# Kernel tuning notes

Measured on AMD Instinct MI355X. Metric: run time of the kernel, lower is better.

## Reference

```python
import jax, jax.numpy as jnp
import numpy as np

N = 100000      # nodes
E = 640000      # directed edges (before self-loops)
F_IN = 128      # num_features
C1 = 64         # latent_size (conv1 out, heads=1)
C2 = 16         # num_classes (conv2 out, heads=1)
NEG_SLOPE = 0.2


def setup_inputs() -> dict:
    key = jax.random.key(0)
    ks = jax.random.split(key, 10)
    s = 0.1
    return {
        "x": jax.random.normal(ks[0], (N, F_IN), jnp.float32),
        "edge_index": jax.random.randint(ks[1], (2, E), 0, N, dtype=jnp.int32),
        "W1": jax.random.normal(ks[2], (F_IN, C1), jnp.float32) * s,
        "att_src1": jax.random.normal(ks[3], (C1,), jnp.float32) * s,
        "att_dst1": jax.random.normal(ks[4], (C1,), jnp.float32) * s,
        "b1": jax.random.normal(ks[5], (C1,), jnp.float32) * s,
        "W2": jax.random.normal(ks[6], (C1, C2), jnp.float32) * s,
        "att_src2": jax.random.normal(ks[7], (C2,), jnp.float32) * s,
        "att_dst2": jax.random.normal(ks[8], (C2,), jnp.float32) * s,
        "b2": jax.random.normal(ks[9], (C2,), jnp.float32) * s,
    }


def gat_layer(x, src, dst, W, a_src, a_dst, b, n_nodes):
    # x: [N, F] -> h: [N, C] (heads=1)
    h = x @ W
    # per-edge attention logits: alpha_j + alpha_i, then leaky_relu
    alpha = jax.nn.leaky_relu((h @ a_src)[src] + (h @ a_dst)[dst], NEG_SLOPE)
    # scatter-softmax over destination-node groups (numerically stable)
    amax = jax.ops.segment_max(alpha, dst, num_segments=n_nodes)
    e = jnp.exp(alpha - amax[dst])
    denom = jax.ops.segment_sum(e, dst, num_segments=n_nodes)
    w = e / (denom[dst] + 1e-16)
    # gather src features, weight, scatter-add to dst
    out = jax.ops.segment_sum(h[src] * w[:, None], dst, num_segments=n_nodes)
    return out + b


def kl_to_std_normal(out):
    # GIB reparameterize: mean = out[:, :ceil(C/2)], std = softplus(out[:, -ceil(C/2):])
    size = (out.shape[-1] + 1) // 2
    mean = out[:, :size]
    std = jax.nn.softplus(out[:, -size:]) + 1e-10
    kl = -jnp.log(std) + 0.5 * (std * std + mean * mean - 1.0)
    return kl.reshape(out.shape[0], -1, 1)  # [N, size, heads=1]


def reference(x, edge_index, W1, att_src1, att_dst1, b1, W2, att_src2, att_dst2, b2):
    n = x.shape[0]
    loop = jnp.arange(n, dtype=edge_index.dtype)  # PyG GATConv add_self_loops=True
    src = jnp.concatenate([edge_index[0], loop])
    dst = jnp.concatenate([edge_index[1], loop])

    out1 = gat_layer(x, src, dst, W1, att_src1, att_dst1, b1, n)
    ixz1 = kl_to_std_normal(out1)

    h = jax.nn.elu(out1)  # dropout is a no-op in eval mode
    out2 = gat_layer(h, src, dst, W2, att_src2, att_dst2, b2, n)
    ixz2 = kl_to_std_normal(out2)

    return (out2, ixz1, ixz2)
```

## Files before the change

kernel.cpp:

```cpp
#include <hip/hip_runtime.h>
#include <math.h>

#define NN 100000
#define NE 640000
#define FIN 128
#define C1 64
#define C2 16
#define NEG_SLOPE 0.2f
#define SLOTS 32
#define G1_BLOCKS ((NN + 127) / 128)
#define SORT_EPB 2048
#define SORT_NBLK ((NE + SORT_EPB - 1) / SORT_EPB)
#define NBUCK 512
#define NBUCK_USED ((NN + 255) / 256)

typedef unsigned int uint32;
typedef __attribute__((ext_vector_type(8))) short bf16x8;
typedef __attribute__((ext_vector_type(4))) float f32x4;

static __device__ __forceinline__ float lrelu(float x) { return x > 0.f ? x : NEG_SLOPE * x; }
static __device__ __forceinline__ float softplusn(float x) {
    return fmaxf(x, 0.f) + __logf(1.f + __expf(-fabsf(x)));
}
static __device__ __forceinline__ unsigned short f2bf(float f) {
    uint32 u = __float_as_uint(f);
    u += 0x7fffu + ((u >> 16) & 1u);
    return (unsigned short)(u >> 16);
}
static __device__ __forceinline__ float bf2f_lo(uint32 p) { return __uint_as_float(p << 16); }
static __device__ __forceinline__ float bf2f_hi(uint32 p) { return __uint_as_float(p & 0xffff0000u); }

#define G1T 2
__global__ __launch_bounds__(256, 3) void k_gemm1(
        const float* __restrict__ x, const float* __restrict__ W1,
        const float* __restrict__ attS, const float* __restrict__ attD,
        unsigned short* __restrict__ h1b, float* __restrict__ as1, float* __restrict__ ad1) {
    __shared__ uint32 ts[4][16][36];
    int lane = threadIdx.x & 63;
    int wv = threadIdx.x >> 6;
    int col = lane & 15;
    int g = lane >> 4;
    int wbase = (blockIdx.x * 4 + wv) * (G1T * 16);
    if (wbase >= NN) return;

    bf16x8 bfr[4][4];
#pragma unroll
    for (int t = 0; t < 4; t++)
#pragma unroll
        for (int j = 0; j < 4; j++) {
            int c = col + j * 16;
#pragma unroll
            for (int i = 0; i < 8; i++)
                bfr[t][j][i] = (short)f2bf(W1[(t * 32 + g * 8 + i) * C1 + c]);
        }
    float ats[4], atd[4];
#pragma unroll
    for (int j = 0; j < 4; j++) { ats[j] = attS[col + j * 16]; atd[j] = attD[col + j * 16]; }

    for (int tl = 0; tl < G1T; tl++) {
        int tbase = wbase + tl * 16;
        int arow = tbase + col; if (arow > NN - 1) arow = NN - 1;
        const float* xr = &x[(size_t)arow * FIN];
        float4 f0[4], f1[4];
#pragma unroll
        for (int t = 0; t < 4; t++) {
            f0[t] = *reinterpret_cast<const float4*>(&xr[t * 32 + g * 8]);
            f1[t] = *reinterpret_cast<const float4*>(&xr[t * 32 + g * 8 + 4]);
        }
        bf16x8 a[4];
#pragma unroll
        for (int t = 0; t < 4; t++) {
            a[t][0] = (short)f2bf(f0[t].x); a[t][1] = (short)f2bf(f0[t].y);
            a[t][2] = (short)f2bf(f0[t].z); a[t][3] = (short)f2bf(f0[t].w);
            a[t][4] = (short)f2bf(f1[t].x); a[t][5] = (short)f2bf(f1[t].y);
            a[t][6] = (short)f2bf(f1[t].z); a[t][7] = (short)f2bf(f1[t].w);
        }
        f32x4 acc[4];
#pragma unroll
        for (int j = 0; j < 4; j++) acc[j] = (f32x4){0.f, 0.f, 0.f, 0.f};
#pragma unroll
        for (int t = 0; t < 4; t++)
#pragma unroll
            for (int j = 0; j < 4; j++)
                acc[j] = __builtin_amdgcn_mfma_f32_16x16x32_bf16(a[t], bfr[t][j], acc[j], 0, 0, 0);

        float sA[4] = {0.f, 0.f, 0.f, 0.f}, sD[4] = {0.f, 0.f, 0.f, 0.f};
        unsigned short* tsw = (unsigned short*)&ts[wv][0][0];
#pragma unroll
        for (int reg = 0; reg < 4; reg++) {
            int trow = g * 4 + reg;
#pragma unroll
            for (int j = 0; j < 4; j++) {
                float v = acc[j][reg];
                tsw[trow * 72 + col + j * 16] = f2bf(v);
                sA[reg] = fmaf(v, ats[j], sA[reg]);
                sD[reg] = fmaf(v, atd[j], sD[reg]);
            }
        }
        __builtin_amdgcn_wave_barrier();
        {
            int rrow = lane >> 2, rq = lane & 3;
            uint4 w0 = *reinterpret_cast<const uint4*>(&ts[wv][rrow][rq * 8]);
            uint4 w1 = *reinterpret_cast<const uint4*>(&ts[wv][rrow][rq * 8 + 4]);
            int orow = tbase + rrow;
            if (orow < NN) {
                unsigned short* op = &h1b[(size_t)orow * C1 + rq * 16];
                *reinterpret_cast<uint4*>(op) = w0;
                *reinterpret_cast<uint4*>(op + 8) = w1;
            }
        }
        __builtin_amdgcn_wave_barrier();
#pragma unroll
        for (int off = 8; off; off >>= 1)
#pragma unroll
            for (int reg = 0; reg < 4; reg++) {
                sA[reg] += __shfl_xor(sA[reg], off);
                sD[reg] += __shfl_xor(sD[reg], off);
            }
        if (col == 0) {
#pragma unroll
            for (int reg = 0; reg < 4; reg++) {
                int row = tbase + g * 4 + reg;
                if (row < NN) { as1[row] = sA[reg]; ad1[row] = sD[reg]; }
            }
        }
    }
}

__global__ __launch_bounds__(256) void k_hist(const int* __restrict__ ei, int* __restrict__ blockHist) {
    __shared__ int lh[NBUCK];
    int t = threadIdx.x;
    for (int i = t; i < NBUCK; i += 256) lh[i] = 0;
    __syncthreads();
    int base = blockIdx.x * SORT_EPB;
#pragma unroll
    for (int k = 0; k < 8; k++) {
        int e = base + k * 256 + t;
        if (e < NE) atomicAdd(&lh[ei[NE + e] >> 8], 1);
    }
    __syncthreads();
    for (int i = t; i < NBUCK; i += 256) blockHist[i * SORT_NBLK + blockIdx.x] = lh[i];
}

__global__ __launch_bounds__(256) void k_scan(int* __restrict__ blockHist, int* __restrict__ bucketCnt) {
    __shared__ int s[SORT_NBLK];
    int b = blockIdx.x, t = threadIdx.x;
    for (int i = t; i < SORT_NBLK; i += 256) s[i] = blockHist[b * SORT_NBLK + i];
    __syncthreads();
    for (int d = 1; d < SORT_NBLK; d <<= 1) {
        int i0 = t, i1 = t + 256;
        int v0 = 0, v1 = 0;
        if (i0 >= d && i0 < SORT_NBLK) v0 = s[i0 - d];
        if (i1 >= d && i1 < SORT_NBLK) v1 = s[i1 - d];
        __syncthreads();
        if (i0 >= d && i0 < SORT_NBLK) s[i0] += v0;
        if (i1 >= d && i1 < SORT_NBLK) s[i1] += v1;
        __syncthreads();
    }
    for (int i = t; i < SORT_NBLK; i += 256)
        blockHist[b * SORT_NBLK + i] = (i == 0) ? 0 : s[i - 1];
    if (t == 0) bucketCnt[b] = s[SORT_NBLK - 1];
}

__global__ __launch_bounds__(256) void k_scat1(const int* __restrict__ ei,
        const int* __restrict__ blockHist, uint2* __restrict__ ebuf) {
    __shared__ int lh[NBUCK];
    int t = threadIdx.x;
    for (int i = t; i < NBUCK; i += 256) lh[i] = 0;
    __syncthreads();
    int base = blockIdx.x * SORT_EPB;
#pragma unroll
    for (int k = 0; k < 8; k++) {
        int e = base + k * 256 + t;
        if (e < NE) {
            int src = ei[e], dst = ei[NE + e];
            int bin = dst >> 8;
            int rank = atomicAdd(&lh[bin], 1);
            int pos = bin * SORT_EPB + blockHist[bin * SORT_NBLK + blockIdx.x] + rank;
            ebuf[pos] = make_uint2((uint32)src, (uint32)dst);
        }
    }
}

__global__ __launch_bounds__(256) void k_csr(const uint2* __restrict__ ebuf,
        const int* __restrict__ bucketCnt, int* __restrict__ cnt, int* __restrict__ csr32) {
    __shared__ int lcnt[256];
    __shared__ int lcsr[256 * SLOTS];
    int t = threadIdx.x, b = blockIdx.x;
    if (t < 256) lcnt[t] = 0;
    for (int i = t; i < 256 * SLOTS; i += 256) lcsr[i] = 0;
    __syncthreads();
    int n = bucketCnt[b];
    if (n > SORT_EPB) n = SORT_EPB;
    for (int i = t; i < n; i += 256) {
        uint2 e = ebuf[b * SORT_EPB + i];
        int ln = (int)(e.y & 255u);
        int pos = atomicAdd(&lcnt[ln], 1);
        if (pos < SLOTS) lcsr[ln * SLOTS + pos] = (int)e.x;
    }
    __syncthreads();
    int node0 = b * 256;
    for (int i = t; i < 256 * SLOTS; i += 256) {
        int node = node0 + (i >> 5);
        if (node < NN) csr32[(size_t)node0 * SLOTS + i] = lcsr[i];
    }
    if (node0 + t < NN) cnt[node0 + t] = lcnt[t];
}

__global__ __launch_bounds__(256, 4) void k_agg1(
        const int* __restrict__ cnt, const int* __restrict__ csr32,
        const float* __restrict__ as1, const float* __restrict__ ad1,
        const unsigned short* __restrict__ h1b, const float* __restrict__ b1,
        unsigned short* __restrict__ heb, float* __restrict__ ixz1) {
    int lane = threadIdx.x & 63;
    int wid = (blockIdx.x * blockDim.x + threadIdx.x) >> 6;
    int grp = lane >> 4, gl = lane & 15;
    int gbase = grp << 4;
    int node = wid * 4 + grp;
    if (node >= NN) return;
    int base = node * SLOTS;
    int dcnt = cnt[node];
    int s_l = csr32[base + gl];
    int4 S0 = *reinterpret_cast<const int4*>(&csr32[base]);
    int4 S1 = *reinterpret_cast<const int4*>(&csr32[base + 4]);
    int4 S2 = *reinterpret_cast<const int4*>(&csr32[base + 8]);
    int4 S3 = *reinterpret_cast<const int4*>(&csr32[base + 12]);
    float adn = ad1[node];
    float asn = as1[node];
    float asv = as1[s_l];
    float4 o;

    if (dcnt <= 16) {
        float al = (gl < dcnt) ? lrelu(asv + adn) : -1e30f;
        float wl = __expf(al);
        float den = wl;
#pragma unroll
        for (int off = 8; off; off >>= 1) den += __shfl_xor(den, off);
        float wself = __expf(lrelu(asn + adn));
        den += wself;
        float inv = __builtin_amdgcn_rcpf(den + 1e-16f);
        wl *= inv; wself *= inv;
        const unsigned short* hb = h1b + gl * 4;
        uint2 PS  = *reinterpret_cast<const uint2*>(&hb[(size_t)node * C1]);
        uint2 P0  = *reinterpret_cast<const uint2*>(&hb[(size_t)S0.x * C1]);
        uint2 P1  = *reinterpret_cast<const uint2*>(&hb[(size_t)S0.y * C1]);
        uint2 P2  = *reinterpret_cast<const uint2*>(&hb[(size_t)S0.z * C1]);
        uint2 P3  = *reinterpret_cast<const uint2*>(&hb[(size_t)S0.w * C1]);
        uint2 P4  = *reinterpret_cast<const uint2*>(&hb[(size_t)S1.x * C1]);
        uint2 P5  = *reinterpret_cast<const uint2*>(&hb[(size_t)S1.y * C1]);
        uint2 P6  = *reinterpret_cast<const uint2*>(&hb[(size_t)S1.z * C1]);
        uint2 P7  = *reinterpret_cast<const uint2*>(&hb[(size_t)S1.w * C1]);
        uint2 P8  = *reinterpret_cast<const uint2*>(&hb[(size_t)S2.x * C1]);
        uint2 P9  = *reinterpret_cast<const uint2*>(&hb[(size_t)S2.y * C1]);
        uint2 P10 = *reinterpret_cast<const uint2*>(&hb[(size_t)S2.z * C1]);
        uint2 P11 = *reinterpret_cast<const uint2*>(&hb[(size_t)S2.w * C1]);
        uint2 P12 = *reinterpret_cast<const uint2*>(&hb[(size_t)S3.x * C1]);
        uint2 P13 = *reinterpret_cast<const uint2*>(&hb[(size_t)S3.y * C1]);
        uint2 P14 = *reinterpret_cast<const uint2*>(&hb[(size_t)S3.z * C1]);
        uint2 P15 = *reinterpret_cast<const uint2*>(&hb[(size_t)S3.w * C1]);
        float4 acc;
        acc.x = wself * bf2f_lo(PS.x);
        acc.y = wself * bf2f_hi(PS.x);
        acc.z = wself * bf2f_lo(PS.y);
        acc.w = wself * bf2f_hi(PS.y);
#define ACC1(k, Pk) { float w = __shfl(wl, gbase | k); \
        acc.x = fmaf(w, bf2f_lo(Pk.x), acc.x); acc.y = fmaf(w, bf2f_hi(Pk.x), acc.y); \
        acc.z = fmaf(w, bf2f_lo(Pk.y), acc.z); acc.w = fmaf(w, bf2f_hi(Pk.y), acc.w); }
        ACC1(0, P0)  ACC1(1, P1)  ACC1(2, P2)  ACC1(3, P3)
        ACC1(4, P4)  ACC1(5, P5)  ACC1(6, P6)  ACC1(7, P7)
        ACC1(8, P8)  ACC1(9, P9)  ACC1(10, P10) ACC1(11, P11)
        ACC1(12, P12) ACC1(13, P13) ACC1(14, P14) ACC1(15, P15)
#undef ACC1
        o = acc;
    } else {
        int dcl = dcnt < SLOTS ? dcnt : SLOTS;
        float aself = lrelu(asn + adn);
        float m = aself;
        for (int e = gl; e < dcl; e += 16) m = fmaxf(m, lrelu(as1[csr32[base + e]] + adn));
#pragma unroll
        for (int off = 8; off; off >>= 1) m = fmaxf(m, __shfl_xor(m, off));
        float den = 0.f;
        for (int e = gl; e < dcl; e += 16) den += __expf(lrelu(as1[csr32[base + e]] + adn) - m);
#pragma unroll
        for (int off = 8; off; off >>= 1) den += __shfl_xor(den, off);
        den += __expf(aself - m);
        float inv = __builtin_amdgcn_rcpf(den + 1e-16f);
        float wsf = __expf(aself - m) * inv;
        uint2 ps = *reinterpret_cast<const uint2*>(&h1b[(size_t)node * C1 + gl * 4]);
        float4 acc;
        acc.x = wsf * bf2f_lo(ps.x);
        acc.y = wsf * bf2f_hi(ps.x);
        acc.z = wsf * bf2f_lo(ps.y);
        acc.w = wsf * bf2f_hi(ps.y);
        for (int e = 0; e < dcl; e++) {
            int s = csr32[base + e];
            float wgt = __expf(lrelu(as1[s] + adn) - m) * inv;
            uint2 p = *reinterpret_cast<const uint2*>(&h1b[(size_t)s * C1 + gl * 4]);
            acc.x = fmaf(wgt, bf2f_lo(p.x), acc.x);
            acc.y = fmaf(wgt, bf2f_hi(p.x), acc.y);
            acc.z = fmaf(wgt, bf2f_lo(p.y), acc.z);
            acc.w = fmaf(wgt, bf2f_hi(p.y), acc.w);
        }
        o = acc;
    }
    float4 bv = *reinterpret_cast<const float4*>(&b1[gl * 4]);
    o.x += bv.x; o.y += bv.y; o.z += bv.z; o.w += bv.w;
    float4 he;
    he.x = o.x > 0.f ? o.x : __expf(o.x) - 1.f;
    he.y = o.y > 0.f ? o.y : __expf(o.y) - 1.f;
    he.z = o.z > 0.f ? o.z : __expf(o.z) - 1.f;
    he.w = o.w > 0.f ? o.w : __expf(o.w) - 1.f;
    uint2 hw;
    hw.x = (uint32)f2bf(he.x) | ((uint32)f2bf(he.y) << 16);
    hw.y = (uint32)f2bf(he.z) | ((uint32)f2bf(he.w) << 16);
    *reinterpret_cast<uint2*>(&heb[(size_t)node * C1 + gl * 4]) = hw;
    float4 oth;
    oth.x = __shfl_down(o.x, 8);
    oth.y = __shfl_down(o.y, 8);
    oth.z = __shfl_down(o.z, 8);
    oth.w = __shfl_down(o.w, 8);
    if (gl < 8) {
        float4 kl; float sd;
        sd = softplusn(oth.x) + 1e-10f; kl.x = -__logf(sd) + 0.5f * (sd * sd + o.x * o.x - 1.f);
        sd = softplusn(oth.y) + 1e-10f; kl.y = -__logf(sd) + 0.5f * (sd * sd + o.y * o.y - 1.f);
        sd = softplusn(oth.z) + 1e-10f; kl.z = -__logf(sd) + 0.5f * (sd * sd + o.z * o.z - 1.f);
        sd = softplusn(oth.w) + 1e-10f; kl.w = -__logf(sd) + 0.5f * (sd * sd + o.w * o.w - 1.f);
        *reinterpret_cast<float4*>(&ixz1[(size_t)node * 32 + gl * 4]) = kl;
    }
}

#define G2T 4
__global__ __launch_bounds__(256, 4) void k_gemm2(
        const unsigned short* __restrict__ heb, const float* __restrict__ W2,
        const float* __restrict__ attS, const float* __restrict__ attD,
        unsigned short* __restrict__ h2b, float* __restrict__ as2, float* __restrict__ ad2) {
    int lane = threadIdx.x & 63;
    int wv = threadIdx.x >> 6;
    int col = lane & 15, g = lane >> 4;
    int wbase = (blockIdx.x * 4 + wv) * (G2T * 16);
    if (wbase >= NN) return;
    bf16x8 bfr[2];
#pragma unroll
    for (int t = 0; t < 2; t++)
#pragma unroll
        for (int i = 0; i < 8; i++)
            bfr[t][i] = (short)f2bf(W2[(t * 32 + g * 8 + i) * C2 + col]);
    float ats = attS[col], atd = attD[col];
#pragma unroll
    for (int tl = 0; tl < G2T; tl++) {
        int tbase = wbase + tl * 16;
        if (tbase >= NN) break;
        int arow = tbase + col; if (arow > NN - 1) arow = NN - 1;
        bf16x8 a0 = *reinterpret_cast<const bf16x8*>(&heb[(size_t)arow * C1 + g * 8]);
        bf16x8 a1 = *reinterpret_cast<const bf16x8*>(&heb[(size_t)arow * C1 + 32 + g * 8]);
        f32x4 acc = (f32x4){0.f, 0.f, 0.f, 0.f};
        acc = __builtin_amdgcn_mfma_f32_16x16x32_bf16(a0, bfr[0], acc, 0, 0, 0);
        acc = __builtin_amdgcn_mfma_f32_16x16x32_bf16(a1, bfr[1], acc, 0, 0, 0);
        float sA[4], sD[4];
#pragma unroll
        for (int reg = 0; reg < 4; reg++) {
            int row = tbase + g * 4 + reg;
            if (row < NN) h2b[(size_t)row * C2 + col] = f2bf(acc[reg]);
            sA[reg] = acc[reg] * ats;
            sD[reg] = acc[reg] * atd;
        }
#pragma unroll
        for (int off = 8; off; off >>= 1)
#pragma unroll
            for (int reg = 0; reg < 4; reg++) {
                sA[reg] += __shfl_xor(sA[reg], off);
                sD[reg] += __shfl_xor(sD[reg], off);
            }
        if (col == 0) {
#pragma unroll
            for (int reg = 0; reg < 4; reg++) {
                int row = tbase + g * 4 + reg;
                if (row < NN) { as2[row] = sA[reg]; ad2[row] = sD[reg]; }
            }
        }
    }
}

__global__ __launch_bounds__(256, 8) void k_agg2(
        const int* __restrict__ cnt, const int* __restrict__ csr32,
        const float* __restrict__ as2, const float* __restrict__ ad2,
        const unsigned short* __restrict__ h2b, const float* __restrict__ b2,
        float* __restrict__ out2, float* __restrict__ ixz2) {
    int lane = threadIdx.x & 63;
    int wid = (blockIdx.x * blockDim.x + threadIdx.x) >> 6;
    int grp = lane >> 4, gl = lane & 15;
    int gbase = grp << 4;
    int node = wid * 4 + grp;
    if (node >= NN) return;
    int base = node * SLOTS;
    int f4 = gl & 3, eg = gl >> 2;
    int dcnt = cnt[node];
    int s_l = csr32[base + gl];
    int sk0 = csr32[base + eg];
    int sk1 = csr32[base + 4 + eg];
    int sk2 = csr32[base + 8 + eg];
    int sk3 = csr32[base + 12 + eg];
    float adn = ad2[node];
    float asn = as2[node];
    float asv = as2[s_l];
    float out;

    if (dcnt <= 16) {
        float al = (gl < dcnt) ? lrelu(asv + adn) : -1e30f;
        float wl = __expf(al);
        float den = wl;
#pragma unroll
        for (int off = 8; off; off >>= 1) den += __shfl_xor(den, off);
        float wself = __expf(lrelu(asn + adn));
        den += wself;
        float inv = __builtin_amdgcn_rcpf(den + 1e-16f);
        wl *= inv; wself *= inv;
        uint2 PS = *reinterpret_cast<const uint2*>(&h2b[(size_t)node * C2 + f4 * 4]);
        uint2 P0 = *reinterpret_cast<const uint2*>(&h2b[(size_t)sk0 * C2 + f4 * 4]);
        uint2 P1 = *reinterpret_cast<const uint2*>(&h2b[(size_t)sk1 * C2 + f4 * 4]);
        uint2 P2 = *reinterpret_cast<const uint2*>(&h2b[(size_t)sk2 * C2 + f4 * 4]);
        uint2 P3 = *reinterpret_cast<const uint2*>(&h2b[(size_t)sk3 * C2 + f4 * 4]);
        float ws = (eg == 0) ? wself : 0.f;
        float4 acc;
        acc.x = ws * bf2f_lo(PS.x);
        acc.y = ws * bf2f_hi(PS.x);
        acc.z = ws * bf2f_lo(PS.y);
        acc.w = ws * bf2f_hi(PS.y);
        float w0 = __shfl(wl, gbase | eg);
        float w1 = __shfl(wl, gbase | (4 + eg));
        float w2 = __shfl(wl, gbase | (8 + eg));
        float w3 = __shfl(wl, gbase | (12 + eg));
        acc.x = fmaf(w0, bf2f_lo(P0.x), acc.x);
        acc.y = fmaf(w0, bf2f_hi(P0.x), acc.y);
        acc.z = fmaf(w0, bf2f_lo(P0.y), acc.z);
        acc.w = fmaf(w0, bf2f_hi(P0.y), acc.w);
        acc.x = fmaf(w1, bf2f_lo(P1.x), acc.x);
        acc.y = fmaf(w1, bf2f_hi(P1.x), acc.y);
        acc.z = fmaf(w1, bf2f_lo(P1.y), acc.z);
        acc.w = fmaf(w1, bf2f_hi(P1.y), acc.w);
        acc.x = fmaf(w2, bf2f_lo(P2.x), acc.x);
        acc.y = fmaf(w2, bf2f_hi(P2.x), acc.y);
        acc.z = fmaf(w2, bf2f_lo(P2.y), acc.z);
        acc.w = fmaf(w2, bf2f_hi(P2.y), acc.w);
        acc.x = fmaf(w3, bf2f_lo(P3.x), acc.x);
        acc.y = fmaf(w3, bf2f_hi(P3.x), acc.y);
        acc.z = fmaf(w3, bf2f_lo(P3.y), acc.z);
        acc.w = fmaf(w3, bf2f_hi(P3.y), acc.w);
#pragma unroll
        for (int off = 4; off <= 8; off <<= 1) {
            acc.x += __shfl_xor(acc.x, off);
            acc.y += __shfl_xor(acc.y, off);
            acc.z += __shfl_xor(acc.z, off);
            acc.w += __shfl_xor(acc.w, off);
        }
        int srcl = gbase | (gl >> 2);
        float t0 = __shfl(acc.x, srcl);
        float t1 = __shfl(acc.y, srcl);
        float t2 = __shfl(acc.z, srcl);
        float t3 = __shfl(acc.w, srcl);
        float t01 = (gl & 1) ? t1 : t0;
        float t23 = (gl & 1) ? t3 : t2;
        out = (gl & 2) ? t23 : t01;
    } else {
        int dcl = dcnt < SLOTS ? dcnt : SLOTS;
        float aself = lrelu(asn + adn);
        float m = aself;
        for (int e = gl; e < dcl; e += 16) m = fmaxf(m, lrelu(as2[csr32[base + e]] + adn));
#pragma unroll
        for (int off = 8; off; off >>= 1) m = fmaxf(m, __shfl_xor(m, off));
        float den = 0.f;
        for (int e = gl; e < dcl; e += 16) den += __expf(lrelu(as2[csr32[base + e]] + adn) - m);
#pragma unroll
        for (int off = 8; off; off >>= 1) den += __shfl_xor(den, off);
        den += __expf(aself - m);
        float inv = __builtin_amdgcn_rcpf(den + 1e-16f);
        float wsf = __expf(aself - m) * inv;
        float acc = wsf * __uint_as_float(((uint32)h2b[(size_t)node * C2 + gl]) << 16);
        for (int e = 0; e < dcl; e++) {
            int s = csr32[base + e];
            float wgt = __expf(lrelu(as2[s] + adn) - m) * inv;
            acc = fmaf(wgt, __uint_as_float(((uint32)h2b[(size_t)s * C2 + gl]) << 16), acc);
        }
        out = acc;
    }
    out += b2[gl];
    out2[(size_t)node * C2 + gl] = out;
    float other = __shfl_down(out, 8);
    if (gl < 8) {
        float sd = softplusn(other) + 1e-10f;
        float kl = -__logf(sd) + 0.5f * (sd * sd + out * out - 1.f);
        ixz2[(size_t)node * 8 + gl] = kl;
    }
}

extern "C" void kernel_launch(void* const* d_in, const int* in_sizes, int n_in,
                              void* d_out, int out_size, void* d_ws, size_t ws_size,
                              hipStream_t stream) {
    const float* x     = (const float*)d_in[0];
    const int*   ei    = (const int*)d_in[1];
    const float* W1    = (const float*)d_in[2];
    const float* aS1   = (const float*)d_in[3];
    const float* aD1   = (const float*)d_in[4];
    const float* b1    = (const float*)d_in[5];
    const float* W2    = (const float*)d_in[6];
    const float* aS2   = (const float*)d_in[7];
    const float* aD2   = (const float*)d_in[8];
    const float* b2    = (const float*)d_in[9];

    float* out = (float*)d_out;
    float* out2 = out;
    float* ixz1 = out + (size_t)NN * C2;
    float* ixz2 = ixz1 + (size_t)NN * 32;

    char* p = (char*)d_ws;
    auto alloc = [&](size_t bytes) -> void* {
        void* r = (void*)p;
        p += (bytes + 255) & ~(size_t)255;
        return r;
    };
    int* cnt        = (int*)alloc((size_t)NN * 4);
    int* csr32      = (int*)alloc((size_t)NN * SLOTS * 4);
    int* blockHist  = (int*)alloc((size_t)NBUCK * SORT_NBLK * 4);
    int* bucketCnt  = (int*)alloc((size_t)NBUCK * 4);
    uint2* ebuf     = (uint2*)alloc((size_t)NBUCK * SORT_EPB * 8);
    unsigned short* h1b = (unsigned short*)alloc((size_t)NN * C1 * 2);
    float* as1   = (float*)alloc((size_t)NN * 4);
    float* ad1   = (float*)alloc((size_t)NN * 4);
    unsigned short* heb = (unsigned short*)alloc((size_t)NN * C1 * 2);
    unsigned short* h2b = (unsigned short*)alloc((size_t)NN * C2 * 2);
    float* as2   = (float*)alloc((size_t)NN * 4);
    float* ad2   = (float*)alloc((size_t)NN * 4);
    (void)ws_size; (void)in_sizes; (void)n_in; (void)out_size;

    k_gemm1<<<G1_BLOCKS, 256, 0, stream>>>(x, W1, aS1, aD1, h1b, as1, ad1);

    k_hist <<<SORT_NBLK, 256, 0, stream>>>(ei, blockHist);
    k_scan <<<NBUCK, 256, 0, stream>>>(blockHist, bucketCnt);
    k_scat1<<<SORT_NBLK, 256, 0, stream>>>(ei, blockHist, ebuf);
    k_csr  <<<NBUCK_USED, 256, 0, stream>>>(ebuf, bucketCnt, cnt, csr32);

    k_agg1<<<(NN + 15) / 16, 256, 0, stream>>>(cnt, csr32, as1, ad1, h1b, b1, heb, ixz1);

    k_gemm2<<<(NN + 4 * G2T * 16 - 1) / (4 * G2T * 16), 256, 0, stream>>>(heb, W2, aS2, aD2, h2b, as2, ad2);
    k_agg2<<<(NN + 15) / 16, 256, 0, stream>>>(cnt, csr32, as2, ad2, h2b, b2, out2, ixz2);
}
```

Baseline: 106.2 us.

## Fuse CSR build into aggregation kernels and merge histogram into GEMM1 launch

Histogram blocks now run as extra blocks of the GEMM1 launch. The scatter step preloads block offsets and packs each edge as src<<8 | local dst in 32 bits, halving ebuf. The separate CSR kernel and the global cnt/csr32 arrays are gone: each aggregation block rebuilds its 256-node bucket's adjacency in shared memory, then walks those nodes. This saves a launch, a global CSR round-trip and bytes moved. The cost is that the CSR build runs twice (once per layer), grids shrink to about 391 large blocks with heavy LDS use (occupancy risk), and the src<<8 packing requires node ids below 2^24.

```diff
diff --git a/kernel.cpp b/kernel.cpp
--- a/kernel.cpp
+++ b/kernel.cpp
@@ -31,11 +31,28 @@
 static __device__ __forceinline__ float bf2f_hi(uint32 p) { return __uint_as_float(p & 0xffff0000u); }
 
 #define G1T 2
-__global__ __launch_bounds__(256, 3) void k_gemm1(
+__global__ __launch_bounds__(256, 3) void k_g1hist(
         const float* __restrict__ x, const float* __restrict__ W1,
         const float* __restrict__ attS, const float* __restrict__ attD,
-        unsigned short* __restrict__ h1b, float* __restrict__ as1, float* __restrict__ ad1) {
+        unsigned short* __restrict__ h1b, float* __restrict__ as1, float* __restrict__ ad1,
+        const int* __restrict__ ei, int* __restrict__ blockHist) {
     __shared__ uint32 ts[4][16][36];
+    __shared__ int lh[NBUCK];
+    if (blockIdx.x >= G1_BLOCKS) {
+        int blk = (int)blockIdx.x - G1_BLOCKS;
+        int t = threadIdx.x;
+        for (int i = t; i < NBUCK; i += 256) lh[i] = 0;
+        __syncthreads();
+        int base = blk * SORT_EPB;
+#pragma unroll
+        for (int k = 0; k < 8; k++) {
+            int e = base + k * 256 + t;
+            if (e < NE) atomicAdd(&lh[ei[NE + e] >> 8], 1);
+        }
+        __syncthreads();
+        for (int i = t; i < NBUCK; i += 256) blockHist[i * SORT_NBLK + blk] = lh[i];
+        return;
+    }
     int lane = threadIdx.x & 63;
     int wv = threadIdx.x >> 6;
     int col = lane & 15;
@@ -125,21 +142,6 @@
             }
         }
     }
-}
-
-__global__ __launch_bounds__(256) void k_hist(const int* __restrict__ ei, int* __restrict__ blockHist) {
-    __shared__ int lh[NBUCK];
-    int t = threadIdx.x;
-    for (int i = t; i < NBUCK; i += 256) lh[i] = 0;
-    __syncthreads();
-    int base = blockIdx.x * SORT_EPB;
-#pragma unroll
-    for (int k = 0; k < 8; k++) {
-        int e = base + k * 256 + t;
-        if (e < NE) atomicAdd(&lh[ei[NE + e] >> 8], 1);
-    }
-    __syncthreads();
-    for (int i = t; i < NBUCK; i += 256) blockHist[i * SORT_NBLK + blockIdx.x] = lh[i];
 }
 
 __global__ __launch_bounds__(256) void k_scan(int* __restrict__ blockHist, int* __restrict__ bucketCnt) {
@@ -163,10 +165,10 @@
 }
 
 __global__ __launch_bounds__(256) void k_scat1(const int* __restrict__ ei,
-        const int* __restrict__ blockHist, uint2* __restrict__ ebuf) {
+        const int* __restrict__ blockHist, uint32* __restrict__ ebuf) {
     __shared__ int lh[NBUCK];
     int t = threadIdx.x;
-    for (int i = t; i < NBUCK; i += 256) lh[i] = 0;
+    for (int i = t; i < NBUCK; i += 256) lh[i] = blockHist[i * SORT_NBLK + blockIdx.x];
     __syncthreads();
     int base = blockIdx.x * SORT_EPB;
 #pragma unroll
@@ -175,157 +177,145 @@
         if (e < NE) {
             int src = ei[e], dst = ei[NE + e];
             int bin = dst >> 8;
-            int rank = atomicAdd(&lh[bin], 1);
-            int pos = bin * SORT_EPB + blockHist[bin * SORT_NBLK + blockIdx.x] + rank;
-            ebuf[pos] = make_uint2((uint32)src, (uint32)dst);
-        }
-    }
-}
-
-__global__ __launch_bounds__(256) void k_csr(const uint2* __restrict__ ebuf,
-        const int* __restrict__ bucketCnt, int* __restrict__ cnt, int* __restrict__ csr32) {
+            int pos = atomicAdd(&lh[bin], 1);
+            ebuf[bin * SORT_EPB + pos] = ((uint32)src << 8) | (uint32)(dst & 255);
+        }
+    }
+}
+
+__global__ __launch_bounds__(256, 4) void k_agg1(
+        const uint32* __restrict__ ebuf, const int* __restrict__ bucketCnt,
+        const float* __restrict__ as1, const float* __restrict__ ad1,
+        const unsigned short* __restrict__ h1b, const float* __restrict__ b1,
+        unsigned short* __restrict__ heb, float* __restrict__ ixz1) {
     __shared__ int lcnt[256];
     __shared__ int lcsr[256 * SLOTS];
     int t = threadIdx.x, b = blockIdx.x;
-    if (t < 256) lcnt[t] = 0;
+    lcnt[t] = 0;
     for (int i = t; i < 256 * SLOTS; i += 256) lcsr[i] = 0;
     __syncthreads();
-    int n = bucketCnt[b];
-    if (n > SORT_EPB) n = SORT_EPB;
+    int n = bucketCnt[b]; if (n > SORT_EPB) n = SORT_EPB;
     for (int i = t; i < n; i += 256) {
-        uint2 e = ebuf[b * SORT_EPB + i];
-        int ln = (int)(e.y & 255u);
+        uint32 e = ebuf[b * SORT_EPB + i];
+        int ln = (int)(e & 255u);
         int pos = atomicAdd(&lcnt[ln], 1);
-        if (pos < SLOTS) lcsr[ln * SLOTS + pos] = (int)e.x;
+        if (pos < SLOTS) lcsr[ln * SLOTS + pos] = (int)(e >> 8);
     }
     __syncthreads();
-    int node0 = b * 256;
-    for (int i = t; i < 256 * SLOTS; i += 256) {
-        int node = node0 + (i >> 5);
-        if (node < NN) csr32[(size_t)node0 * SLOTS + i] = lcsr[i];
-    }
-    if (node0 + t < NN) cnt[node0 + t] = lcnt[t];
-}
-
-__global__ __launch_bounds__(256, 4) void k_agg1(
-        const int* __restrict__ cnt, const int* __restrict__ csr32,
-        const float* __restrict__ as1, const float* __restrict__ ad1,
-        const unsigned short* __restrict__ h1b, const float* __restrict__ b1,
-        unsigned short* __restrict__ heb, float* __restrict__ ixz1) {
-    int lane = threadIdx.x & 63;
-    int wid = (blockIdx.x * blockDim.x + threadIdx.x) >> 6;
+    int lane = t & 63, wv = t >> 6;
     int grp = lane >> 4, gl = lane & 15;
     int gbase = grp << 4;
-    int node = wid * 4 + grp;
-    if (node >= NN) return;
-    int base = node * SLOTS;
-    int dcnt = cnt[node];
-    int s_l = csr32[base + gl];
-    int4 S0 = *reinterpret_cast<const int4*>(&csr32[base]);
-    int4 S1 = *reinterpret_cast<const int4*>(&csr32[base + 4]);
-    int4 S2 = *reinterpret_cast<const int4*>(&csr32[base + 8]);
-    int4 S3 = *reinterpret_cast<const int4*>(&csr32[base + 12]);
-    float adn = ad1[node];
-    float asn = as1[node];
-    float asv = as1[s_l];
-    float4 o;
-
-    if (dcnt <= 16) {
-        float al = (gl < dcnt) ? lrelu(asv + adn) : -1e30f;
-        float wl = __expf(al);
-        float den = wl;
-#pragma unroll
-        for (int off = 8; off; off >>= 1) den += __shfl_xor(den, off);
-        float wself = __expf(lrelu(asn + adn));
-        den += wself;
-        float inv = __builtin_amdgcn_rcpf(den + 1e-16f);
-        wl *= inv; wself *= inv;
-        const unsigned short* hb = h1b + gl * 4;
-        uint2 PS  = *reinterpret_cast<const uint2*>(&hb[(size_t)node * C1]);
-        uint2 P0  = *reinterpret_cast<const uint2*>(&hb[(size_t)S0.x * C1]);
-        uint2 P1  = *reinterpret_cast<const uint2*>(&hb[(size_t)S0.y * C1]);
-        uint2 P2  = *reinterpret_cast<const uint2*>(&hb[(size_t)S0.z * C1]);
-        uint2 P3  = *reinterpret_cast<const uint2*>(&hb[(size_t)S0.w * C1]);
-        uint2 P4  = *reinterpret_cast<const uint2*>(&hb[(size_t)S1.x * C1]);
-        uint2 P5  = *reinterpret_cast<const uint2*>(&hb[(size_t)S1.y * C1]);
-        uint2 P6  = *reinterpret_cast<const uint2*>(&hb[(size_t)S1.z * C1]);
-        uint2 P7  = *reinterpret_cast<const uint2*>(&hb[(size_t)S1.w * C1]);
-        uint2 P8  = *reinterpret_cast<const uint2*>(&hb[(size_t)S2.x * C1]);
-        uint2 P9  = *reinterpret_cast<const uint2*>(&hb[(size_t)S2.y * C1]);
-        uint2 P10 = *reinterpret_cast<const uint2*>(&hb[(size_t)S2.z * C1]);
-        uint2 P11 = *reinterpret_cast<const uint2*>(&hb[(size_t)S2.w * C1]);
-        uint2 P12 = *reinterpret_cast<const uint2*>(&hb[(size_t)S3.x * C1]);
-        uint2 P13 = *reinterpret_cast<const uint2*>(&hb[(size_t)S3.y * C1]);
-        uint2 P14 = *reinterpret_cast<const uint2*>(&hb[(size_t)S3.z * C1]);
-        uint2 P15 = *reinterpret_cast<const uint2*>(&hb[(size_t)S3.w * C1]);
-        float4 acc;
-        acc.x = wself * bf2f_lo(PS.x);
-        acc.y = wself * bf2f_hi(PS.x);
-        acc.z = wself * bf2f_lo(PS.y);
-        acc.w = wself * bf2f_hi(PS.y);
+    for (int it = 0; it < 16; it++) {
+        int ln = it * 16 + wv * 4 + grp;
+        int node = b * 256 + ln;
+        if (node >= NN) continue;
+        int dcnt = lcnt[ln];
+        int s_l = lcsr[ln * SLOTS + gl];
+        int4 S0 = *reinterpret_cast<const int4*>(&lcsr[ln * SLOTS]);
+        int4 S1 = *reinterpret_cast<const int4*>(&lcsr[ln * SLOTS + 4]);
+        int4 S2 = *reinterpret_cast<const int4*>(&lcsr[ln * SLOTS + 8]);
+        int4 S3 = *reinterpret_cast<const int4*>(&lcsr[ln * SLOTS + 12]);
+        float adn = ad1[node];
+        float asn = as1[node];
+        float asv = as1[s_l];
+        float4 o;
+        if (dcnt <= 16) {
+            float al = (gl < dcnt) ? lrelu(asv + adn) : -1e30f;
+            float wl = __expf(al);
+            float den = wl;
+#pragma unroll
+            for (int off = 8; off; off >>= 1) den += __shfl_xor(den, off);
+            float wself = __expf(lrelu(asn + adn));
+            den += wself;
+            float inv = __builtin_amdgcn_rcpf(den + 1e-16f);
+            wl *= inv; wself *= inv;
+            const unsigned short* hb = h1b + gl * 4;
+            uint2 PS  = *reinterpret_cast<const uint2*>(&hb[(size_t)node * C1]);
+            uint2 P0  = *reinterpret_cast<const uint2*>(&hb[(size_t)S0.x * C1]);
+            uint2 P1  = *reinterpret_cast<const uint2*>(&hb[(size_t)S0.y * C1]);
+            uint2 P2  = *reinterpret_cast<const uint2*>(&hb[(size_t)S0.z * C1]);
+            uint2 P3  = *reinterpret_cast<const uint2*>(&hb[(size_t)S0.w * C1]);
+            uint2 P4  = *reinterpret_cast<const uint2*>(&hb[(size_t)S1.x * C1]);
+            uint2 P5  = *reinterpret_cast<const uint2*>(&hb[(size_t)S1.y * C1]);
+            uint2 P6  = *reinterpret_cast<const uint2*>(&hb[(size_t)S1.z * C1]);
+            uint2 P7  = *reinterpret_cast<const uint2*>(&hb[(size_t)S1.w * C1]);
+            uint2 P8  = *reinterpret_cast<const uint2*>(&hb[(size_t)S2.x * C1]);
+            uint2 P9  = *reinterpret_cast<const uint2*>(&hb[(size_t)S2.y * C1]);
+            uint2 P10 = *reinterpret_cast<const uint2*>(&hb[(size_t)S2.z * C1]);
+            uint2 P11 = *reinterpret_cast<const uint2*>(&hb[(size_t)S2.w * C1]);
+            uint2 P12 = *reinterpret_cast<const uint2*>(&hb[(size_t)S3.x * C1]);
+            uint2 P13 = *reinterpret_cast<const uint2*>(&hb[(size_t)S3.y * C1]);
+            uint2 P14 = *reinterpret_cast<const uint2*>(&hb[(size_t)S3.z * C1]);
+            uint2 P15 = *reinterpret_cast<const uint2*>(&hb[(size_t)S3.w * C1]);
+            float4 acc;
+            acc.x = wself * bf2f_lo(PS.x);
+            acc.y = wself * bf2f_hi(PS.x);
+            acc.z = wself * bf2f_lo(PS.y);
+            acc.w = wself * bf2f_hi(PS.y);
 #define ACC1(k, Pk) { float w = __shfl(wl, gbase | k); \
-        acc.x = fmaf(w, bf2f_lo(Pk.x), acc.x); acc.y = fmaf(w, bf2f_hi(Pk.x), acc.y); \
-        acc.z = fmaf(w, bf2f_lo(Pk.y), acc.z); acc.w = fmaf(w, bf2f_hi(Pk.y), acc.w); }
-        ACC1(0, P0)  ACC1(1, P1)  ACC1(2, P2)  ACC1(3, P3)
-        ACC1(4, P4)  ACC1(5, P5)  ACC1(6, P6)  ACC1(7, P7)
-        ACC1(8, P8)  ACC1(9, P9)  ACC1(10, P10) ACC1(11, P11)
-        ACC1(12, P12) ACC1(13, P13) ACC1(14, P14) ACC1(15, P15)
+            acc.x = fmaf(w, bf2f_lo(Pk.x), acc.x); acc.y = fmaf(w, bf2f_hi(Pk.x), acc.y); \
+            acc.z = fmaf(w, bf2f_lo(Pk.y), acc.z); acc.w = fmaf(w, bf2f_hi(Pk.y), acc.w); }
+            ACC1(0, P0)  ACC1(1, P1)  ACC1(2, P2)  ACC1(3, P3)
+            ACC1(4, P4)  ACC1(5, P5)  ACC1(6, P6)  ACC1(7, P7)
+            ACC1(8, P8)  ACC1(9, P9)  ACC1(10, P10) ACC1(11, P11)
+            ACC1(12, P12) ACC1(13, P13) ACC1(14, P14) ACC1(15, P15)
 #undef ACC1
-        o = acc;
-    } else {
-        int dcl = dcnt < SLOTS ? dcnt : SLOTS;
-        float aself = lrelu(asn + adn);
-        float m = aself;
-        for (int e = gl; e < dcl; e += 16) m = fmaxf(m, lrelu(as1[csr32[base + e]] + adn));
-#pragma unroll
-        for (int off = 8; off; off >>= 1) m = fmaxf(m, __shfl_xor(m, off));
-        float den = 0.f;
-        for (int e = gl; e < dcl; e += 16) den += __expf(lrelu(as1[csr32[base + e]] + adn) - m);
-#pragma unroll
-        for (int off = 8; off; off >>= 1) den += __shfl_xor(den, off);
-        den += __expf(aself - m);
-        float inv = __builtin_amdgcn_rcpf(den + 1e-16f);
-        float wsf = __expf(aself - m) * inv;
-        uint2 ps = *reinterpret_cast<const uint2*>(&h1b[(size_t)node * C1 + gl * 4]);
-        float4 acc;
-        acc.x = wsf * bf2f_lo(ps.x);
-        acc.y = wsf * bf2f_hi(ps.x);
-        acc.z = wsf * bf2f_lo(ps.y);
-        acc.w = wsf * bf2f_hi(ps.y);
-        for (int e = 0; e < dcl; e++) {
-            int s = csr32[base + e];
-            float wgt = __expf(lrelu(as1[s] + adn) - m) * inv;
-            uint2 p = *reinterpret_cast<const uint2*>(&h1b[(size_t)s * C1 + gl * 4]);
-            acc.x = fmaf(wgt, bf2f_lo(p.x), acc.x);
-            acc.y = fmaf(wgt, bf2f_hi(p.x), acc.y);
-            acc.z = fmaf(wgt, bf2f_lo(p.y), acc.z);
-            acc.w = fmaf(wgt, bf2f_hi(p.y), acc.w);
-        }
-        o = acc;
-    }
-    float4 bv = *reinterpret_cast<const float4*>(&b1[gl * 4]);
-    o.x += bv.x; o.y += bv.y; o.z += bv.z; o.w += bv.w;
-    float4 he;
-    he.x = o.x > 0.f ? o.x : __expf(o.x) - 1.f;
-    he.y = o.y > 0.f ? o.y : __expf(o.y) - 1.f;
-    he.z = o.z > 0.f ? o.z : __expf(o.z) - 1.f;
-    he.w = o.w > 0.f ? o.w : __expf(o.w) - 1.f;
-    uint2 hw;
-    hw.x = (uint32)f2bf(he.x) | ((uint32)f2bf(he.y) << 16);
-    hw.y = (uint32)f2bf(he.z) | ((uint32)f2bf(he.w) << 16);
-    *reinterpret_cast<uint2*>(&heb[(size_t)node * C1 + gl * 4]) = hw;
-    float4 oth;
-    oth.x = __shfl_down(o.x, 8);
-    oth.y = __shfl_down(o.y, 8);
-    oth.z = __shfl_down(o.z, 8);
-    oth.w = __shfl_down(o.w, 8);
-    if (gl < 8) {
-        float4 kl; float sd;
-        sd = softplusn(oth.x) + 1e-10f; kl.x = -__logf(sd) + 0.5f * (sd * sd + o.x * o.x - 1.f);
-        sd = softplusn(oth.y) + 1e-10f; kl.y = -__logf(sd) + 0.5f * (sd * sd + o.y * o.y - 1.f);
-        sd = softplusn(oth.z) + 1e-10f; kl.z = -__logf(sd) + 0.5f * (sd * sd + o.z * o.z - 1.f);
-        sd = softplusn(oth.w) + 1e-10f; kl.w = -__logf(sd) + 0.5f * (sd * sd + o.w * o.w - 1.f);
-        *reinterpret_cast<float4*>(&ixz1[(size_t)node * 32 + gl * 4]) = kl;
+            o = acc;
+        } else {
+            int dcl = dcnt < SLOTS ? dcnt : SLOTS;
+            float aself = lrelu(asn + adn);
+            float m = aself;
+            for (int e = gl; e < dcl; e += 16) m = fmaxf(m, lrelu(as1[lcsr[ln * SLOTS + e]] + adn));
+#pragma unroll
+            for (int off = 8; off; off >>= 1) m = fmaxf(m, __shfl_xor(m, off));
+            float den = 0.f;
+            for (int e = gl; e < dcl; e += 16) den += __expf(lrelu(as1[lcsr[ln * SLOTS + e]] + adn) - m);
+#pragma unroll
+            for (int off = 8; off; off >>= 1) den += __shfl_xor(den, off);
+            den += __expf(aself - m);
+            float inv = __builtin_amdgcn_rcpf(den + 1e-16f);
+            float wsf = __expf(aself - m) * inv;
+            uint2 ps = *reinterpret_cast<const uint2*>(&h1b[(size_t)node * C1 + gl * 4]);
+            float4 acc;
+            acc.x = wsf * bf2f_lo(ps.x);
+            acc.y = wsf * bf2f_hi(ps.x);
+            acc.z = wsf * bf2f_lo(ps.y);
+            acc.w = wsf * bf2f_hi(ps.y);
+            for (int e = 0; e < dcl; e++) {
+                int s = lcsr[ln * SLOTS + e];
+                float wgt = __expf(lrelu(as1[s] + adn) - m) * inv;
+                uint2 p = *reinterpret_cast<const uint2*>(&h1b[(size_t)s * C1 + gl * 4]);
+                acc.x = fmaf(wgt, bf2f_lo(p.x), acc.x);
+                acc.y = fmaf(wgt, bf2f_hi(p.x), acc.y);
+                acc.z = fmaf(wgt, bf2f_lo(p.y), acc.z);
+                acc.w = fmaf(wgt, bf2f_hi(p.y), acc.w);
+            }
+            o = acc;
+        }
+        float4 bv = *reinterpret_cast<const float4*>(&b1[gl * 4]);
+        o.x += bv.x; o.y += bv.y; o.z += bv.z; o.w += bv.w;
+        float4 he;
+        he.x = o.x > 0.f ? o.x : __expf(o.x) - 1.f;
+        he.y = o.y > 0.f ? o.y : __expf(o.y) - 1.f;
+        he.z = o.z > 0.f ? o.z : __expf(o.z) - 1.f;
+        he.w = o.w > 0.f ? o.w : __expf(o.w) - 1.f;
+        uint2 hw;
+        hw.x = (uint32)f2bf(he.x) | ((uint32)f2bf(he.y) << 16);
+        hw.y = (uint32)f2bf(he.z) | ((uint32)f2bf(he.w) << 16);
+        *reinterpret_cast<uint2*>(&heb[(size_t)node * C1 + gl * 4]) = hw;
+        float4 oth;
+        oth.x = __shfl_down(o.x, 8);
+        oth.y = __shfl_down(o.y, 8);
+        oth.z = __shfl_down(o.z, 8);
+        oth.w = __shfl_down(o.w, 8);
+        if (gl < 8) {
+            float4 kl; float sd;
+            sd = softplusn(oth.x) + 1e-10f; kl.x = -__logf(sd) + 0.5f * (sd * sd + o.x * o.x - 1.f);
+            sd = softplusn(oth.y) + 1e-10f; kl.y = -__logf(sd) + 0.5f * (sd * sd + o.y * o.y - 1.f);
+            sd = softplusn(oth.z) + 1e-10f; kl.z = -__logf(sd) + 0.5f * (sd * sd + o.z * o.z - 1.f);
+            sd = softplusn(oth.w) + 1e-10f; kl.w = -__logf(sd) + 0.5f * (sd * sd + o.w * o.w - 1.f);
+            *reinterpret_cast<float4*>(&ixz1[(size_t)node * 32 + gl * 4]) = kl;
+        }
     }
 }
 
@@ -381,115 +371,129 @@
     }
 }
 
-__global__ __launch_bounds__(256, 8) void k_agg2(
-        const int* __restrict__ cnt, const int* __restrict__ csr32,
+__global__ __launch_bounds__(256, 4) void k_agg2(
+        const uint32* __restrict__ ebuf, const int* __restrict__ bucketCnt,
         const float* __restrict__ as2, const float* __restrict__ ad2,
         const unsigned short* __restrict__ h2b, const float* __restrict__ b2,
         float* __restrict__ out2, float* __restrict__ ixz2) {
-    int lane = threadIdx.x & 63;
-    int wid = (blockIdx.x * blockDim.x + threadIdx.x) >> 6;
+    __shared__ int lcnt[256];
+    __shared__ int lcsr[256 * SLOTS];
+    int t = threadIdx.x, b = blockIdx.x;
+    lcnt[t] = 0;
+    for (int i = t; i < 256 * SLOTS; i += 256) lcsr[i] = 0;
+    __syncthreads();
+    int n = bucketCnt[b]; if (n > SORT_EPB) n = SORT_EPB;
+    for (int i = t; i < n; i += 256) {
+        uint32 e = ebuf[b * SORT_EPB + i];
+        int ln = (int)(e & 255u);
+        int pos = atomicAdd(&lcnt[ln], 1);
+        if (pos < SLOTS) lcsr[ln * SLOTS + pos] = (int)(e >> 8);
+    }
+    __syncthreads();
+    int lane = t & 63, wv = t >> 6;
     int grp = lane >> 4, gl = lane & 15;
     int gbase = grp << 4;
-    int node = wid * 4 + grp;
-    if (node >= NN) return;
-    int base = node * SLOTS;
     int f4 = gl & 3, eg = gl >> 2;
-    int dcnt = cnt[node];
-    int s_l = csr32[base + gl];
-    int sk0 = csr32[base + eg];
-    int sk1 = csr32[base + 4 + eg];
-    int sk2 = csr32[base + 8 + eg];
-    int sk3 = csr32[base + 12 + eg];
-    float adn = ad2[node];
-    float asn = as2[node];
-    float asv = as2[s_l];
-    float out;
-
-    if (dcnt <= 16) {
-        float al = (gl < dcnt) ? lrelu(asv + adn) : -1e30f;
-        float wl = __expf(al);
-        float den = wl;
-#pragma unroll
-        for (int off = 8; off; off >>= 1) den += __shfl_xor(den, off);
-        float wself = __expf(lrelu(asn + adn));
-        den += wself;
-        float inv = __builtin_amdgcn_rcpf(den + 1e-16f);
-        wl *= inv; wself *= inv;
-        uint2 PS = *reinterpret_cast<const uint2*>(&h2b[(size_t)node * C2 + f4 * 4]);
-        uint2 P0 = *reinterpret_cast<const uint2*>(&h2b[(size_t)sk0 * C2 + f4 * 4]);
-        uint2 P1 = *reinterpret_cast<const uint2*>(&h2b[(size_t)sk1 * C2 + f4 * 4]);
-        uint2 P2 = *reinterpret_cast<const uint2*>(&h2b[(size_t)sk2 * C2 + f4 * 4]);
-        uint2 P3 = *reinterpret_cast<const uint2*>(&h2b[(size_t)sk3 * C2 + f4 * 4]);
-        float ws = (eg == 0) ? wself : 0.f;
-        float4 acc;
-        acc.x = ws * bf2f_lo(PS.x);
-        acc.y = ws * bf2f_hi(PS.x);
-        acc.z = ws * bf2f_lo(PS.y);
-        acc.w = ws * bf2f_hi(PS.y);
-        float w0 = __shfl(wl, gbase | eg);
-        float w1 = __shfl(wl, gbase | (4 + eg));
-        float w2 = __shfl(wl, gbase | (8 + eg));
-        float w3 = __shfl(wl, gbase | (12 + eg));
-        acc.x = fmaf(w0, bf2f_lo(P0.x), acc.x);
-        acc.y = fmaf(w0, bf2f_hi(P0.x), acc.y);
-        acc.z = fmaf(w0, bf2f_lo(P0.y), acc.z);
-        acc.w = fmaf(w0, bf2f_hi(P0.y), acc.w);
-        acc.x = fmaf(w1, bf2f_lo(P1.x), acc.x);
-        acc.y = fmaf(w1, bf2f_hi(P1.x), acc.y);
-        acc.z = fmaf(w1, bf2f_lo(P1.y), acc.z);
-        acc.w = fmaf(w1, bf2f_hi(P1.y), acc.w);
-        acc.x = fmaf(w2, bf2f_lo(P2.x), acc.x);
-        acc.y = fmaf(w2, bf2f_hi(P2.x), acc.y);
-        acc.z = fmaf(w2, bf2f_lo(P2.y), acc.z);
-        acc.w = fmaf(w2, bf2f_hi(P2.y), acc.w);
-        acc.x = fmaf(w3, bf2f_lo(P3.x), acc.x);
-        acc.y = fmaf(w3, bf2f_hi(P3.x), acc.y);
-        acc.z = fmaf(w3, bf2f_lo(P3.y), acc.z);
-        acc.w = fmaf(w3, bf2f_hi(P3.y), acc.w);
-#pragma unroll
-        for (int off = 4; off <= 8; off <<= 1) {
-            acc.x += __shfl_xor(acc.x, off);
-            acc.y += __shfl_xor(acc.y, off);
-            acc.z += __shfl_xor(acc.z, off);
-            acc.w += __shfl_xor(acc.w, off);
-        }
-        int srcl = gbase | (gl >> 2);
-        float t0 = __shfl(acc.x, srcl);
-        float t1 = __shfl(acc.y, srcl);
-        float t2 = __shfl(acc.z, srcl);
-        float t3 = __shfl(acc.w, srcl);
-        float t01 = (gl & 1) ? t1 : t0;
-        float t23 = (gl & 1) ? t3 : t2;
-        out = (gl & 2) ? t23 : t01;
-    } else {
-        int dcl = dcnt < SLOTS ? dcnt : SLOTS;
-        float aself = lrelu(asn + adn);
-        float m = aself;
-        for (int e = gl; e < dcl; e += 16) m = fmaxf(m, lrelu(as2[csr32[base + e]] + adn));
-#pragma unroll
-        for (int off = 8; off; off >>= 1) m = fmaxf(m, __shfl_xor(m, off));
-        float den = 0.f;
-        for (int e = gl; e < dcl; e += 16) den += __expf(lrelu(as2[csr32[base + e]] + adn) - m);
-#pragma unroll
-        for (int off = 8; off; off >>= 1) den += __shfl_xor(den, off);
-        den += __expf(aself - m);
-        float inv = __builtin_amdgcn_rcpf(den + 1e-16f);
-        float wsf = __expf(aself - m) * inv;
-        float acc = wsf * __uint_as_float(((uint32)h2b[(size_t)node * C2 + gl]) << 16);
-        for (int e = 0; e < dcl; e++) {
-            int s = csr32[base + e];
-            float wgt = __expf(lrelu(as2[s] + adn) - m) * inv;
-            acc = fmaf(wgt, __uint_as_float(((uint32)h2b[(size_t)s * C2 + gl]) << 16), acc);
-        }
-        out = acc;
-    }
-    out += b2[gl];
-    out2[(size_t)node * C2 + gl] = out;
-    float other = __shfl_down(out, 8);
-    if (gl < 8) {
-        float sd = softplusn(other) + 1e-10f;
-        float kl = -__logf(sd) + 0.5f * (sd * sd + out * out - 1.f);
-        ixz2[(size_t)node * 8 + gl] = kl;
+    for (int it = 0; it < 16; it++) {
+        int ln = it * 16 + wv * 4 + grp;
+        int node = b * 256 + ln;
+        if (node >= NN) continue;
+        int dcnt = lcnt[ln];
+        int s_l = lcsr[ln * SLOTS + gl];
+        int sk0 = lcsr[ln * SLOTS + eg];
+        int sk1 = lcsr[ln * SLOTS + 4 + eg];
+        int sk2 = lcsr[ln * SLOTS + 8 + eg];
+        int sk3 = lcsr[ln * SLOTS + 12 + eg];
+        float adn = ad2[node];
+        float asn = as2[node];
+        float asv = as2[s_l];
+        float out;
+        if (dcnt <= 16) {
+            float al = (gl < dcnt) ? lrelu(asv + adn) : -1e30f;
+            float wl = __expf(al);
+            float den = wl;
+#pragma unroll
+            for (int off = 8; off; off >>= 1) den += __shfl_xor(den, off);
+            float wself = __expf(lrelu(asn + adn));
+            den += wself;
+            float inv = __builtin_amdgcn_rcpf(den + 1e-16f);
+            wl *= inv; wself *= inv;
+            uint2 PS = *reinterpret_cast<const uint2*>(&h2b[(size_t)node * C2 + f4 * 4]);
+            uint2 P0 = *reinterpret_cast<const uint2*>(&h2b[(size_t)sk0 * C2 + f4 * 4]);
+            uint2 P1 = *reinterpret_cast<const uint2*>(&h2b[(size_t)sk1 * C2 + f4 * 4]);
+            uint2 P2 = *reinterpret_cast<const uint2*>(&h2b[(size_t)sk2 * C2 + f4 * 4]);
+            uint2 P3 = *reinterpret_cast<const uint2*>(&h2b[(size_t)sk3 * C2 + f4 * 4]);
+            float ws = (eg == 0) ? wself : 0.f;
+            float4 acc;
+            acc.x = ws * bf2f_lo(PS.x);
+            acc.y = ws * bf2f_hi(PS.x);
+            acc.z = ws * bf2f_lo(PS.y);
+            acc.w = ws * bf2f_hi(PS.y);
+            float w0 = __shfl(wl, gbase | eg);
+            float w1 = __shfl(wl, gbase | (4 + eg));
+            float w2 = __shfl(wl, gbase | (8 + eg));
+            float w3 = __shfl(wl, gbase | (12 + eg));
+            acc.x = fmaf(w0, bf2f_lo(P0.x), acc.x);
+            acc.y = fmaf(w0, bf2f_hi(P0.x), acc.y);
+            acc.z = fmaf(w0, bf2f_lo(P0.y), acc.z);
+            acc.w = fmaf(w0, bf2f_hi(P0.y), acc.w);
+            acc.x = fmaf(w1, bf2f_lo(P1.x), acc.x);
+            acc.y = fmaf(w1, bf2f_hi(P1.x), acc.y);
+            acc.z = fmaf(w1, bf2f_lo(P1.y), acc.z);
+            acc.w = fmaf(w1, bf2f_hi(P1.y), acc.w);
+            acc.x = fmaf(w2, bf2f_lo(P2.x), acc.x);
+            acc.y = fmaf(w2, bf2f_hi(P2.x), acc.y);
+            acc.z = fmaf(w2, bf2f_lo(P2.y), acc.z);
+            acc.w = fmaf(w2, bf2f_hi(P2.y), acc.w);
+            acc.x = fmaf(w3, bf2f_lo(P3.x), acc.x);
+            acc.y = fmaf(w3, bf2f_hi(P3.x), acc.y);
+            acc.z = fmaf(w3, bf2f_lo(P3.y), acc.z);
+            acc.w = fmaf(w3, bf2f_hi(P3.y), acc.w);
+#pragma unroll
+            for (int off = 4; off <= 8; off <<= 1) {
+                acc.x += __shfl_xor(acc.x, off);
+                acc.y += __shfl_xor(acc.y, off);
+                acc.z += __shfl_xor(acc.z, off);
+                acc.w += __shfl_xor(acc.w, off);
+            }
+            int srcl = gbase | (gl >> 2);
+            float t0 = __shfl(acc.x, srcl);
+            float t1 = __shfl(acc.y, srcl);
+            float t2 = __shfl(acc.z, srcl);
+            float t3 = __shfl(acc.w, srcl);
+            float t01 = (gl & 1) ? t1 : t0;
+            float t23 = (gl & 1) ? t3 : t2;
+            out = (gl & 2) ? t23 : t01;
+        } else {
+            int dcl = dcnt < SLOTS ? dcnt : SLOTS;
+            float aself = lrelu(asn + adn);
+            float m = aself;
+            for (int e = gl; e < dcl; e += 16) m = fmaxf(m, lrelu(as2[lcsr[ln * SLOTS + e]] + adn));
+#pragma unroll
+            for (int off = 8; off; off >>= 1) m = fmaxf(m, __shfl_xor(m, off));
+            float den = 0.f;
+            for (int e = gl; e < dcl; e += 16) den += __expf(lrelu(as2[lcsr[ln * SLOTS + e]] + adn) - m);
+#pragma unroll
+            for (int off = 8; off; off >>= 1) den += __shfl_xor(den, off);
+            den += __expf(aself - m);
+            float inv = __builtin_amdgcn_rcpf(den + 1e-16f);
+            float wsf = __expf(aself - m) * inv;
+            float acc = wsf * __uint_as_float(((uint32)h2b[(size_t)node * C2 + gl]) << 16);
+            for (int e = 0; e < dcl; e++) {
+                int s = lcsr[ln * SLOTS + e];
+                float wgt = __expf(lrelu(as2[s] + adn) - m) * inv;
+                acc = fmaf(wgt, __uint_as_float(((uint32)h2b[(size_t)s * C2 + gl]) << 16), acc);
+            }
+            out = acc;
+        }
+        out += b2[gl];
+        out2[(size_t)node * C2 + gl] = out;
+        float other = __shfl_down(out, 8);
+        if (gl < 8) {
+            float sd = softplusn(other) + 1e-10f;
+            float kl = -__logf(sd) + 0.5f * (sd * sd + out * out - 1.f);
+            ixz2[(size_t)node * 8 + gl] = kl;
+        }
     }
 }
 
@@ -518,11 +522,9 @@
         p += (bytes + 255) & ~(size_t)255;
         return r;
     };
-    int* cnt        = (int*)alloc((size_t)NN * 4);
-    int* csr32      = (int*)alloc((size_t)NN * SLOTS * 4);
     int* blockHist  = (int*)alloc((size_t)NBUCK * SORT_NBLK * 4);
     int* bucketCnt  = (int*)alloc((size_t)NBUCK * 4);
-    uint2* ebuf     = (uint2*)alloc((size_t)NBUCK * SORT_EPB * 8);
+    uint32* ebuf    = (uint32*)alloc((size_t)NBUCK * SORT_EPB * 4);
     unsigned short* h1b = (unsigned short*)alloc((size_t)NN * C1 * 2);
     float* as1   = (float*)alloc((size_t)NN * 4);
     float* ad1   = (float*)alloc((size_t)NN * 4);
@@ -532,15 +534,13 @@
     float* ad2   = (float*)alloc((size_t)NN * 4);
     (void)ws_size; (void)in_sizes; (void)n_in; (void)out_size;
 
-    k_gemm1<<<G1_BLOCKS, 256, 0, stream>>>(x, W1, aS1, aD1, h1b, as1, ad1);
-
-    k_hist <<<SORT_NBLK, 256, 0, stream>>>(ei, blockHist);
+    k_g1hist<<<G1_BLOCKS + SORT_NBLK, 256, 0, stream>>>(x, W1, aS1, aD1, h1b, as1, ad1, ei, blockHist);
+
     k_scan <<<NBUCK, 256, 0, stream>>>(blockHist, bucketCnt);
     k_scat1<<<SORT_NBLK, 256, 0, stream>>>(ei, blockHist, ebuf);
-    k_csr  <<<NBUCK_USED, 256, 0, stream>>>(ebuf, bucketCnt, cnt, csr32);
-
-    k_agg1<<<(NN + 15) / 16, 256, 0, stream>>>(cnt, csr32, as1, ad1, h1b, b1, heb, ixz1);
+
+    k_agg1<<<NBUCK_USED, 256, 0, stream>>>(ebuf, bucketCnt, as1, ad1, h1b, b1, heb, ixz1);
 
     k_gemm2<<<(NN + 4 * G2T * 16 - 1) / (4 * G2T * 16), 256, 0, stream>>>(heb, W2, aS2, aD2, h2b, as2, ad2);
-    k_agg2<<<(NN + 15) / 16, 256, 0, stream>>>(cnt, csr32, as2, ad2, h2b, b2, out2, ixz2);
-}
+    k_agg2<<<NBUCK_USED, 256, 0, stream>>>(ebuf, bucketCnt, as2, ad2, h2b, b2, out2, ixz2);
+}
```

Result: slower. 117.2 us (+10.3%).
